# Kernel optimization log

Hardware: AMD Instinct MI355X
Metric: run time of the kernel (lower is better)

The kernel has to match this reference:

```python
import jax, jax.numpy as jnp
import numpy as np

D_MODEL = 512
HEADS = 8
FF_HIDDEN = 1024
EPS = 1e-6


def setup_inputs() -> dict:
    key = jax.random.key(0)
    ks = jax.random.split(key, 12)
    s = 1.0 / np.sqrt(D_MODEL)
    inp = {
        'x': jax.random.normal(ks[0], (2, 4096, D_MODEL), dtype=jnp.float32),
        'Wq': jax.random.normal(ks[1], (D_MODEL, D_MODEL), dtype=jnp.float32) * s,
        'bq': jnp.zeros((D_MODEL,), jnp.float32),
        'Wk': jax.random.normal(ks[2], (D_MODEL, D_MODEL), dtype=jnp.float32) * s,
        'bk': jnp.zeros((D_MODEL,), jnp.float32),
        'Wv': jax.random.normal(ks[3], (D_MODEL, D_MODEL), dtype=jnp.float32) * s,
        'bv': jnp.zeros((D_MODEL,), jnp.float32),
        'Wo': jax.random.normal(ks[4], (D_MODEL, D_MODEL), dtype=jnp.float32) * s,
        'bo': jnp.zeros((D_MODEL,), jnp.float32),
        'a1': jnp.ones((D_MODEL,), jnp.float32),
        'b1': jnp.zeros((D_MODEL,), jnp.float32),
        'a2': jnp.ones((D_MODEL,), jnp.float32),
        'b2': jnp.zeros((D_MODEL,), jnp.float32),
        'W1': jax.random.normal(ks[5], (D_MODEL, FF_HIDDEN), dtype=jnp.float32) * s,
        'c1': jnp.zeros((FF_HIDDEN,), jnp.float32),
        'W2': jax.random.normal(ks[6], (FF_HIDDEN, D_MODEL), dtype=jnp.float32) * (1.0 / np.sqrt(FF_HIDDEN)),
        'c2': jnp.zeros((D_MODEL,), jnp.float32),
    }
    return inp


def _layer_norm(x, a, b):
    # Faithful to source: uses unbiased std (torch default) and divides by (std + eps)
    mean = jnp.mean(x, axis=-1, keepdims=True)
    std = jnp.std(x, axis=-1, keepdims=True, ddof=1)
    return a * ((x - mean) / (std + EPS)) + b


def _encoder_block(x, Wq, bq, Wk, bk, Wv, bv, Wo, bo, a1, b1, a2, b2, W1, c1, W2, c2):
    B, S, D = x.shape
    H, dk = HEADS, D // HEADS
    q = (x @ Wq + bq).reshape(B, S, H, dk).transpose(0, 2, 1, 3)  # [B,H,S,dk]
    k = (x @ Wk + bk).reshape(B, S, H, dk).transpose(0, 2, 1, 3)
    v = (x @ Wv + bv).reshape(B, S, H, dk).transpose(0, 2, 1, 3)
    scores = jnp.einsum('bhqd,bhkd->bhqk', q, k) / np.sqrt(dk)
    probs = jax.nn.softmax(scores, axis=-1)
    attn = jnp.einsum('bhqk,bhkd->bhqd', probs, v)
    concat = attn.transpose(0, 2, 1, 3).reshape(B, S, D)
    attn_out = concat @ Wo + bo
    x = _layer_norm(x + attn_out, a1, b1)  # dropout = identity (eval mode)
    ffn = jax.nn.relu(x @ W1 + c1) @ W2 + c2
    return _layer_norm(x + ffn, a2, b2)


def reference(x, Wq, bq, Wk, bk, Wv, bv, Wo, bo, a1, b1, a2, b2, W1, c1, W2, c2):
    return _encoder_block(x, Wq, bq, Wk, bk, Wv, bv, Wo, bo, a1, b1, a2, b2, W1, c1, W2, c2)
```

## Files before the change

### kernel.cpp

```cpp
#include <hip/hip_runtime.h>
#include <stdint.h>

typedef short short8 __attribute__((ext_vector_type(8)));
typedef short short4v __attribute__((ext_vector_type(4)));
typedef float f32x4 __attribute__((ext_vector_type(4)));
typedef float f32x16 __attribute__((ext_vector_type(16)));
typedef unsigned int u32x4 __attribute__((ext_vector_type(4)));

#define LOG2E 1.44269504088896f
#define QSCALE (0.125f * LOG2E)

__device__ __forceinline__ unsigned short f2b(float f) {
  union { float f; unsigned int u; } x; x.f = f;
  unsigned int u = x.u;
  unsigned int r = (u + 0x7fffu + ((u >> 16) & 1u)) >> 16;
  return (unsigned short)r;
}
__device__ __forceinline__ float b2f(unsigned short s) {
  union { unsigned int u; float f; } x; x.u = ((unsigned int)s) << 16;
  return x.f;
}
__device__ __forceinline__ void gl16(const void* g, void* l) {
  __builtin_amdgcn_global_load_lds((const __attribute__((address_space(1))) void*)g,
                                   (__attribute__((address_space(3))) void*)l, 16, 0, 0);
}
__device__ __forceinline__ unsigned int cvtpk(float lo, float hi) {
  unsigned int r;
  asm("v_cvt_pk_bf16_f32 %0, %1, %2" : "=v"(r) : "v"(lo), "v"(hi));
  return r;
}
__device__ __forceinline__ void plswap(unsigned int& a, unsigned int& b) {
  asm volatile("v_permlane32_swap_b32 %0, %1" : "+v"(a), "+v"(b));
}

__global__ __launch_bounds__(256) void prep_k(
    const float* __restrict__ X, unsigned short* __restrict__ Xb,
    const float* __restrict__ Wq, const float* __restrict__ Wk,
    const float* __restrict__ Wv, const float* __restrict__ Wo,
    const float* __restrict__ W1, const float* __restrict__ W2,
    unsigned short* __restrict__ WqkvT, unsigned short* __restrict__ WoT,
    unsigned short* __restrict__ W1T, unsigned short* __restrict__ W2T,
    const float* __restrict__ bq, const float* __restrict__ bk,
    const float* __restrict__ bv, float* __restrict__ Bqkv) {
  __shared__ float t[64][65];
  int bid = blockIdx.x, tid = threadIdx.x;
  if (bid < 2048) {
    int i = bid * 256 + tid;
    const float* p = X + (size_t)i * 8;
    float4 a = *(const float4*)(p);
    float4 b = *(const float4*)(p + 4);
    short8 o;
    o[0] = (short)f2b(a.x); o[1] = (short)f2b(a.y);
    o[2] = (short)f2b(a.z); o[3] = (short)f2b(a.w);
    o[4] = (short)f2b(b.x); o[5] = (short)f2b(b.y);
    o[6] = (short)f2b(b.z); o[7] = (short)f2b(b.w);
    *(short8*)(Xb + (size_t)i * 8) = o;
    return;
  }
  if (bid == 2560) {
    for (int i = tid; i < 1536; i += 256) {
      float v = (i < 512) ? bq[i] * QSCALE : (i < 1024 ? bk[i - 512] : bv[i - 1024]);
      Bqkv[i] = v;
    }
    return;
  }
  int idx = bid - 2048;
  const float* W; unsigned short* WT; int K, N, kb, nb; float scale = 1.0f;
  if (idx < 256) {
    int sec = idx >> 6, local = idx & 63;
    K = 512; N = 512; kb = local >> 3; nb = local & 7;
    if (sec == 0) { W = Wq; WT = WqkvT; scale = QSCALE; }
    else if (sec == 1) { W = Wk; WT = WqkvT + 512 * 512; }
    else if (sec == 2) { W = Wv; WT = WqkvT + 2 * 512 * 512; }
    else { W = Wo; WT = WoT; }
  } else if (idx < 384) {
    int local = idx - 256; K = 512; N = 1024; kb = local >> 4; nb = local & 15;
    W = W1; WT = W1T;
  } else {
    int local = idx - 384; K = 1024; N = 512; kb = local >> 3; nb = local & 7;
    W = W2; WT = W2T;
  }
  int k0 = kb * 64, n0 = nb * 64;
  for (int i = tid; i < 4096; i += 256) {
    int r = i >> 6, c = i & 63;
    t[r][c] = W[(size_t)(k0 + r) * N + n0 + c];
  }
  __syncthreads();
  for (int i = tid; i < 4096; i += 256) {
    int r = i >> 6, c = i & 63;
    WT[(size_t)(n0 + r) * K + k0 + c] = f2b(t[c][r] * scale);
  }
}

template <int EPI>
__global__ __launch_bounds__(256) void gemm_bt(
    const unsigned short* __restrict__ A, const unsigned short* __restrict__ BT,
    const float* __restrict__ bias, float* __restrict__ Cf,
    unsigned short* __restrict__ Cb, int M, int N, int K) {
  __shared__ unsigned short As[2][128 * 32];
  __shared__ unsigned short Bs[2][128 * 32];
  int t = threadIdx.x, w = t >> 6, l = t & 63;
  int linb = blockIdx.x + gridDim.x * blockIdx.y;
  int q8 = (gridDim.x * gridDim.y) >> 3;
  int wk = (linb & 7) * q8 + (linb >> 3);
  int bm = wk / gridDim.y, bn = wk % gridDim.y;
  int wm = w >> 1, wn = w & 1;
  int g = l >> 4, ln = l & 15;
  f32x4 acc[4][4] = {};
  const unsigned short* Arow = A + (size_t)bm * 128 * K;
  const unsigned short* Brow = BT + (size_t)bn * 128 * K;
  int nk = K >> 5;

  auto stageg = [&](int buf, int kt) {
    int k0 = kt * 32;
#pragma unroll
    for (int i = 0; i < 2; ++i) {
      int cl = i * 256 + t;
      int r = cl >> 2, c = cl & 3;
      char* ldsA = (char*)&As[buf][0] + (size_t)(i * 256 + w * 64) * 16;
      char* ldsB = (char*)&Bs[buf][0] + (size_t)(i * 256 + w * 64) * 16;
      gl16(Arow + (size_t)r * K + k0 + c * 8, ldsA);
      gl16(Brow + (size_t)r * K + k0 + c * 8, ldsB);
    }
  };

  stageg(0, 0);
  for (int kt = 0; kt < nk; ++kt) {
    int cur = kt & 1;
    if (kt + 1 < nk) {
      stageg(cur ^ 1, kt + 1);
      asm volatile("s_waitcnt vmcnt(4)" ::: "memory");
    } else {
      asm volatile("s_waitcnt vmcnt(0)" ::: "memory");
    }
    __builtin_amdgcn_s_barrier();
    __builtin_amdgcn_sched_barrier(0);
    short8 af[4], bf[4];
    int ko = g * 8;
#pragma unroll
    for (int i = 0; i < 4; ++i)
      af[i] = *(const short8*)&As[cur][(wm * 64 + i * 16 + ln) * 32 + ko];
#pragma unroll
    for (int j = 0; j < 4; ++j)
      bf[j] = *(const short8*)&Bs[cur][(wn * 64 + j * 16 + ln) * 32 + ko];
    __builtin_amdgcn_s_setprio(1);
#pragma unroll
    for (int i = 0; i < 4; ++i)
#pragma unroll
      for (int j = 0; j < 4; ++j)
        acc[i][j] = __builtin_amdgcn_mfma_f32_16x16x32_bf16(af[i], bf[j], acc[i][j], 0, 0, 0);
    __builtin_amdgcn_s_setprio(0);
    __builtin_amdgcn_s_barrier();
  }
#pragma unroll
  for (int i = 0; i < 4; ++i) {
    int row = bm * 128 + wm * 64 + i * 16 + g * 4;
#pragma unroll
    for (int j = 0; j < 4; ++j) {
      int col = bn * 128 + wn * 64 + j * 16 + ln;
      float bv = bias[col];
      float vv[4];
#pragma unroll
      for (int r = 0; r < 4; ++r) {
        float v = acc[i][j][r] + bv;
        if constexpr (EPI == 2) v = v > 0.f ? v : 0.f;
        vv[r] = v;
      }
      if constexpr (EPI == 3) {
        if (col < 1024) {
#pragma unroll
          for (int r = 0; r < 4; ++r)
            Cb[(size_t)(col >> 9) * 4194304 + (size_t)(row + r) * 512 + (col & 511)] = f2b(vv[r]);
        } else {
          short4v pk;
#pragma unroll
          for (int r = 0; r < 4; ++r) pk[r] = (short)f2b(vv[r]);
          *(short4v*)((unsigned short*)Cf +
                      (size_t)((row >> 12) * 512 + (col & 511)) * 4096 + (row & 4095)) = pk;
        }
      } else {
#pragma unroll
        for (int r = 0; r < 4; ++r)
          Cb[(size_t)(row + r) * N + col] = f2b(vv[r]);
      }
    }
  }
}

template <int AMODE, bool WB>
__global__ __launch_bounds__(512) void gemmln_k(
    const unsigned short* __restrict__ A, const unsigned short* __restrict__ BT,
    const float* __restrict__ bias, const float* __restrict__ X,
    const float* __restrict__ gamma, const float* __restrict__ beta,
    float* __restrict__ outf, unsigned short* __restrict__ outb,
    const unsigned short* __restrict__ Opart, const float* __restrict__ L,
    int K) {
  __shared__ unsigned short As[AMODE ? 32 * 520 : 2 * 32 * 32];
  __shared__ unsigned short Bs[2][512 * 32];
  __shared__ float stats[8][32][2];
  __shared__ float minv[32][2];
  __shared__ float sli[8][32];
  int tid = threadIdx.x, wv = tid >> 6, lane = tid & 63;
  int g = lane >> 4, ln = lane & 15;
  int bm = blockIdx.x;
  int row0 = bm * 32;
  f32x4 acc[2][4] = {};

  if constexpr (AMODE == 1) {
    int b = row0 >> 12;
    int q0 = row0 & 4095;
    if (tid < 256) {
      int h = tid >> 5, qq = tid & 31;
      int bh = b * 8 + h;
      float s = L[(size_t)bh * 4096 + q0 + qq] + L[(size_t)(16 + bh) * 4096 + q0 + qq];
      sli[h][qq] = 1.0f / s;
    }
    __syncthreads();
    int col = tid;
    int h = col >> 6, d = col & 63;
    int bh = b * 8 + h;
    const unsigned short* p0 = Opart + (size_t)bh * 262144 + (size_t)d * 4096 + q0;
    const unsigned short* p1 = Opart + (size_t)(16 + bh) * 262144 + (size_t)d * 4096 + q0;
#pragma unroll
    for (int i = 0; i < 4; ++i) {
      short8 a = *(const short8*)(p0 + i * 8);
      short8 c = *(const short8*)(p1 + i * 8);
#pragma unroll
      for (int j = 0; j < 8; ++j) {
        int qq = i * 8 + j;
        float s = (b2f((unsigned short)a[j]) + b2f((unsigned short)c[j])) * sli[h][qq];
        As[qq * 520 + col] = f2b(s);
      }
    }
    __syncthreads();
  }

  const unsigned short* Arow = (AMODE == 0) ? (A + (size_t)bm * 32 * K) : nullptr;
  int nk = K >> 5;

  auto stageg = [&](int buf, int kt) {
    int k0 = kt * 32;
    if constexpr (AMODE == 0) {
      if (tid < 128) {
        int r = tid >> 2, c = tid & 3;
        gl16(Arow + (size_t)r * K + k0 + c * 8, (char*)As + (size_t)buf * 2048 + tid * 16);
      }
    }
#pragma unroll
    for (int i = 0; i < 4; ++i) {
      int u = i * 512 + tid;
      int r = u >> 2, c = u & 3;
      gl16(BT + (size_t)r * K + k0 + c * 8, (char*)&Bs[buf][0] + (size_t)u * 16);
    }
  };

  stageg(0, 0);
  for (int kt = 0; kt < nk; ++kt) {
    int cur = kt & 1;
    if (kt + 1 < nk) {
      stageg(cur ^ 1, kt + 1);
      if constexpr (AMODE == 0) {
        if (wv < 2) asm volatile("s_waitcnt vmcnt(5)" ::: "memory");
        else        asm volatile("s_waitcnt vmcnt(4)" ::: "memory");
      } else {
        asm volatile("s_waitcnt vmcnt(4)" ::: "memory");
      }
    } else {
      asm volatile("s_waitcnt vmcnt(0)" ::: "memory");
    }
    __builtin_amdgcn_s_barrier();
    __builtin_amdgcn_sched_barrier(0);
    int k0 = kt * 32;
    short8 af[2], bf[4];
#pragma unroll
    for (int i = 0; i < 2; ++i) {
      if constexpr (AMODE == 1)
        af[i] = *(const short8*)&As[(i * 16 + ln) * 520 + k0 + g * 8];
      else
        af[i] = *(const short8*)&As[cur * 1024 + (i * 16 + ln) * 32 + g * 8];
    }
#pragma unroll
    for (int j = 0; j < 4; ++j)
      bf[j] = *(const short8*)&Bs[cur][(wv * 64 + j * 16 + ln) * 32 + g * 8];
    __builtin_amdgcn_s_setprio(1);
#pragma unroll
    for (int i = 0; i < 2; ++i)
#pragma unroll
      for (int j = 0; j < 4; ++j)
        acc[i][j] = __builtin_amdgcn_mfma_f32_16x16x32_bf16(af[i], bf[j], acc[i][j], 0, 0, 0);
    __builtin_amdgcn_s_setprio(0);
    __builtin_amdgcn_s_barrier();
  }
  float v[2][4][4];
  float ps[8], pss[8];
#pragma unroll
  for (int k = 0; k < 8; ++k) { ps[k] = 0.f; pss[k] = 0.f; }
#pragma unroll
  for (int i = 0; i < 2; ++i)
#pragma unroll
    for (int j = 0; j < 4; ++j) {
      int col = wv * 64 + j * 16 + ln;
      float bv = bias[col];
#pragma unroll
      for (int r = 0; r < 4; ++r) {
        int row = i * 16 + g * 4 + r;
        float t = acc[i][j][r] + bv + X[(size_t)(row0 + row) * 512 + col];
        v[i][j][r] = t;
        ps[i * 4 + r] += t; pss[i * 4 + r] += t * t;
      }
    }
#pragma unroll
  for (int off = 1; off < 16; off <<= 1) {
#pragma unroll
    for (int k = 0; k < 8; ++k) {
      ps[k] += __shfl_xor(ps[k], off);
      pss[k] += __shfl_xor(pss[k], off);
    }
  }
  if (ln == 0) {
#pragma unroll
    for (int i = 0; i < 2; ++i)
#pragma unroll
      for (int r = 0; r < 4; ++r) {
        stats[wv][i * 16 + g * 4 + r][0] = ps[i * 4 + r];
        stats[wv][i * 16 + g * 4 + r][1] = pss[i * 4 + r];
      }
  }
  __syncthreads();
  if (tid < 32) {
    float S = 0.f, SS = 0.f;
#pragma unroll
    for (int w2 = 0; w2 < 8; ++w2) { S += stats[w2][tid][0]; SS += stats[w2][tid][1]; }
    float mean = S * (1.f / 512.f);
    float var = fmaxf((SS - 512.f * mean * mean) * (1.f / 511.f), 0.f);
    minv[tid][0] = mean;
    minv[tid][1] = 1.f / (sqrtf(var) + 1e-6f);
  }
  __syncthreads();
#pragma unroll
  for (int i = 0; i < 2; ++i)
#pragma unroll
    for (int j = 0; j < 4; ++j) {
      int col = wv * 64 + j * 16 + ln;
      float gm = gamma[col], bt2 = beta[col];
#pragma unroll
      for (int r = 0; r < 4; ++r) {
        int row = i * 16 + g * 4 + r;
        float o = gm * ((v[i][j][r] - minv[row][0]) * minv[row][1]) + bt2;
        outf[(size_t)(row0 + row) * 512 + col] = o;
        if constexpr (WB) outb[(size_t)(row0 + row) * 512 + col] = f2b(o);
      }
    }
}

__global__ __launch_bounds__(256, 2) void attn_k(
    const unsigned short* __restrict__ Q, const unsigned short* __restrict__ Kb,
    const unsigned short* __restrict__ Vt, unsigned short* __restrict__ Opart,
    float* __restrict__ L) {
  __shared__ unsigned short Ks[2][4096];
  __shared__ unsigned short Vs[3][4096];
  int tid = threadIdx.x, wv = tid >> 6, lane = tid & 63;
  int l31 = lane & 31, hi = lane >> 5;
  int lin = blockIdx.x + 16 * blockIdx.y + 256 * blockIdx.z;
  int wk = (lin & 7) * 64 + (lin >> 3);
  int qb = wk & 15, bh = (wk >> 4) & 15, z = wk >> 8;
  int b = bh >> 3, h = bh & 7;
  int q0 = qb * 256 + wv * 64;
  int kvbase = z * 2048;

  short8 qfA[4], qfB[4];
  {
    const unsigned short* qpA = Q + (size_t)(b * 4096 + q0 + l31) * 512 + h * 64;
    const unsigned short* qpB = qpA + 32 * 512;
#pragma unroll
    for (int ks = 0; ks < 4; ++ks) {
      qfA[ks] = *(const short8*)(qpA + ks * 16 + hi * 8);
      qfB[ks] = *(const short8*)(qpB + ks * 16 + hi * 8);
    }
  }

  short8 ones;
#pragma unroll
  for (int j = 0; j < 8; ++j) ones[j] = (short)0x3F80;

  const f32x16 Z = {};
  f32x16 oA0 = {}, oA1 = {}, oB0 = {}, oB1 = {}, laccA = {}, laccB = {};

  int skk[2], sc[2];
#pragma unroll
  for (int i = 0; i < 2; ++i) {
    int u = i * 256 + tid;
    int r2 = u >> 4, s = u & 15;
    skk[i] = 2 * r2 + (s & 1);
    sc[i] = ((s >> 1) ^ (r2 & 7)) * 8;
  }

  auto stage = [&](char* kb_lds, char* vb_lds, int kv) {
    const unsigned short* ksrc = Kb + (size_t)(b * 4096 + kv) * 512 + h * 64;
    const unsigned short* vsrc = Vt + (size_t)(bh * 64) * 4096 + kv;
#pragma unroll
    for (int i = 0; i < 2; ++i) {
      gl16(ksrc + (size_t)skk[i] * 512 + sc[i], kb_lds + (size_t)(i * 256 + wv * 64) * 16);
      gl16(vsrc + (size_t)skk[i] * 4096 + sc[i], vb_lds + (size_t)(i * 256 + wv * 64) * 16);
    }
  };

  int r2a = l31 >> 1, par = l31 & 1, perm = r2a & 7;
  int rdb = r2a * 256 + (par << 4);

  auto qk = [&](const char* kbase, f32x16& sA0, f32x16& sA1, f32x16& sB0, f32x16& sB1) {
    __builtin_amdgcn_s_setprio(1);
#pragma unroll
    for (int ks = 0; ks < 4; ++ks) {
      int c16 = ks * 2 + hi;
      int byteA = rdb + (((c16 ^ perm) << 1) << 4);
      short8 k0 = *(const short8*)(kbase + byteA);
      short8 k1 = *(const short8*)(kbase + byteA + 4096);
      if (ks == 0) {
        sA0 = __builtin_amdgcn_mfma_f32_32x32x16_bf16(k0, qfA[0], Z, 0, 0, 0);
        sA1 = __builtin_amdgcn_mfma_f32_32x32x16_bf16(k1, qfA[0], Z, 0, 0, 0);
        sB0 = __builtin_amdgcn_mfma_f32_32x32x16_bf16(k0, qfB[0], Z, 0, 0, 0);
        sB1 = __builtin_amdgcn_mfma_f32_32x32x16_bf16(k1, qfB[0], Z, 0, 0, 0);
      } else {
        sA0 = __builtin_amdgcn_mfma_f32_32x32x16_bf16(k0, qfA[ks], sA0, 0, 0, 0);
        sA1 = __builtin_amdgcn_mfma_f32_32x32x16_bf16(k1, qfA[ks], sA1, 0, 0, 0);
        sB0 = __builtin_amdgcn_mfma_f32_32x32x16_bf16(k0, qfB[ks], sB0, 0, 0, 0);
        sB1 = __builtin_amdgcn_mfma_f32_32x32x16_bf16(k1, qfB[ks], sB1, 0, 0, 0);
      }
    }
    __builtin_amdgcn_s_setprio(0);
  };

  auto pv = [&](const char* vbase, const short8* pfA, const short8* pfB) {
    __builtin_amdgcn_s_setprio(1);
#pragma unroll
    for (int ks = 0; ks < 4; ++ks) {
      int c16 = ks * 2 + hi;
      int byteA = rdb + (((c16 ^ perm) << 1) << 4);
      short8 v0 = *(const short8*)(vbase + byteA);
      short8 v1 = *(const short8*)(vbase + byteA + 4096);
      oA0 = __builtin_amdgcn_mfma_f32_32x32x16_bf16(v0, pfA[ks], oA0, 0, 0, 0);
      oA1 = __builtin_amdgcn_mfma_f32_32x32x16_bf16(v1, pfA[ks], oA1, 0, 0, 0);
      oB0 = __builtin_amdgcn_mfma_f32_32x32x16_bf16(v0, pfB[ks], oB0, 0, 0, 0);
      oB1 = __builtin_amdgcn_mfma_f32_32x32x16_bf16(v1, pfB[ks], oB1, 0, 0, 0);
      laccA = __builtin_amdgcn_mfma_f32_32x32x16_bf16(ones, pfA[ks], laccA, 0, 0, 0);
      laccB = __builtin_amdgcn_mfma_f32_32x32x16_bf16(ones, pfB[ks], laccB, 0, 0, 0);
    }
    __builtin_amdgcn_s_setprio(0);
  };

  auto exppack = [&](f32x16& s0, f32x16& s1, short8* pf) {
#pragma unroll
    for (int r = 0; r < 16; ++r) s0[r] = __builtin_amdgcn_exp2f(s0[r]);
#pragma unroll
    for (int r = 0; r < 16; ++r) s1[r] = __builtin_amdgcn_exp2f(s1[r]);
    unsigned int u0 = cvtpk(s0[0], s0[1]), u1 = cvtpk(s0[4], s0[5]);
    plswap(u0, u1);
    unsigned int u2 = cvtpk(s0[2], s0[3]), u3 = cvtpk(s0[6], s0[7]);
    plswap(u2, u3);
    unsigned int u4 = cvtpk(s0[8], s0[9]), u5 = cvtpk(s0[12], s0[13]);
    plswap(u4, u5);
    unsigned int u6 = cvtpk(s0[10], s0[11]), u7 = cvtpk(s0[14], s0[15]);
    plswap(u6, u7);
    union { u32x4 u; short8 s; } cv;
    cv.u = (u32x4){u0, u2, u1, u3}; pf[0] = cv.s;
    cv.u = (u32x4){u4, u6, u5, u7}; pf[1] = cv.s;
    unsigned int w0 = cvtpk(s1[0], s1[1]), w1 = cvtpk(s1[4], s1[5]);
    plswap(w0, w1);
    unsigned int w2 = cvtpk(s1[2], s1[3]), w3 = cvtpk(s1[6], s1[7]);
    plswap(w2, w3);
    unsigned int w4 = cvtpk(s1[8], s1[9]), w5 = cvtpk(s1[12], s1[13]);
    plswap(w4, w5);
    unsigned int w6 = cvtpk(s1[10], s1[11]), w7 = cvtpk(s1[14], s1[15]);
    plswap(w6, w7);
    cv.u = (u32x4){w0, w2, w1, w3}; pf[2] = cv.s;
    cv.u = (u32x4){w4, w6, w5, w7}; pf[3] = cv.s;
  };

  char* k0b = (char*)&Ks[0][0];
  char* k1b = (char*)&Ks[1][0];
  char* vA = (char*)&Vs[0][0];
  char* vB = (char*)&Vs[1][0];
  char* vC = (char*)&Vs[2][0];
  stage(k0b, vA, kvbase);
  __syncthreads();
  stage(k1b, vB, kvbase + 64);

  f32x16 sA0, sA1, sB0, sB1;
  qk(k0b, sA0, sA1, sB0, sB1);
  short8 pfA[4], pfB[4];
  exppack(sA0, sA1, pfA);
  exppack(sB0, sB1, pfB);

#pragma unroll 1
  for (int t = 1; t < 32; ++t) {
    __syncthreads();
    char* kr = (t & 1) ? k1b : k0b;
    char* kw = (t & 1) ? k0b : k1b;
    if (t < 31) stage(kw, vC, kvbase + (t + 1) * 64);
    qk(kr, sA0, sA1, sB0, sB1);
    pv(vA, pfA, pfB);
    exppack(sA0, sA1, pfA);
    exppack(sB0, sB1, pfB);
    char* tmp = vA; vA = vB; vB = vC; vC = tmp;
  }
  pv(vA, pfA, pfB);

  int plane = z * 16 + bh;
  unsigned short* op = Opart + (size_t)plane * 262144;
  int qA = q0 + l31, qB = q0 + 32 + l31;
#pragma unroll
  for (int r = 0; r < 16; ++r) {
    int dr = (r & 3) + 8 * (r >> 2) + 4 * hi;
    op[(size_t)dr * 4096 + qA] = f2b(oA0[r]);
    op[(size_t)(dr + 32) * 4096 + qA] = f2b(oA1[r]);
    op[(size_t)dr * 4096 + qB] = f2b(oB0[r]);
    op[(size_t)(dr + 32) * 4096 + qB] = f2b(oB1[r]);
  }
  if (hi == 0) {
    L[(size_t)plane * 4096 + qA] = laccA[0];
    L[(size_t)plane * 4096 + qB] = laccB[0];
  }
}

extern "C" void kernel_launch(void* const* d_in, const int* in_sizes, int n_in,
                              void* d_out, int out_size, void* d_ws, size_t ws_size,
                              hipStream_t stream) {
  const float* x  = (const float*)d_in[0];
  const float* Wq = (const float*)d_in[1];
  const float* bq = (const float*)d_in[2];
  const float* Wk = (const float*)d_in[3];
  const float* bk = (const float*)d_in[4];
  const float* Wv = (const float*)d_in[5];
  const float* bv = (const float*)d_in[6];
  const float* Wo = (const float*)d_in[7];
  const float* bo = (const float*)d_in[8];
  const float* a1 = (const float*)d_in[9];
  const float* b1 = (const float*)d_in[10];
  const float* a2 = (const float*)d_in[11];
  const float* b2 = (const float*)d_in[12];
  const float* W1 = (const float*)d_in[13];
  const float* c1 = (const float*)d_in[14];
  const float* W2 = (const float*)d_in[15];
  const float* c2 = (const float*)d_in[16];

  char* ws = (char*)d_ws;
  const size_t MB = 1024 * 1024;
  unsigned short* Xb  = (unsigned short*)(ws + 0);
  unsigned short* Qb  = (unsigned short*)(ws + 8 * MB);
  unsigned short* Kbf = (unsigned short*)(ws + 16 * MB);
  float* L = (float*)(ws + 24 * MB);
  unsigned short* Vtb = (unsigned short*)(ws + 32 * MB);
  unsigned short* WqkvT = (unsigned short*)(ws + 40 * MB);
  unsigned short* WoT = (unsigned short*)(ws + 41 * MB + 512 * 1024);
  unsigned short* W1T = (unsigned short*)(ws + 42 * MB);
  unsigned short* W2T = (unsigned short*)(ws + 43 * MB);
  unsigned short* Opart = (unsigned short*)(ws + 44 * MB);
  float* Bqkv = (float*)(ws + 44 * MB);
  float* Y1 = (float*)(ws + 60 * MB);
  unsigned short* Y1b = Qb;
  unsigned short* Hb  = Kbf;

  prep_k<<<2561, 256, 0, stream>>>(x, Xb, Wq, Wk, Wv, Wo, W1, W2,
                                   WqkvT, WoT, W1T, W2T, bq, bk, bv, Bqkv);

  gemm_bt<3><<<dim3(64, 12), 256, 0, stream>>>(Xb, WqkvT, Bqkv, (float*)Vtb, Qb, 8192, 1536, 512);

  attn_k<<<dim3(16, 16, 2), 256, 0, stream>>>(Qb, Kbf, Vtb, Opart, L);

  gemmln_k<1, true><<<256, 512, 0, stream>>>(nullptr, WoT, bo, x, a1, b1, Y1, Y1b,
                                             Opart, L, 512);
  gemm_bt<2><<<dim3(64, 8), 256, 0, stream>>>(Y1b, W1T, c1, nullptr, Hb, 8192, 1024, 512);
  gemmln_k<0, false><<<256, 512, 0, stream>>>(Hb, W2T, c2, Y1, a2, b2, (float*)d_out, nullptr,
                                              nullptr, nullptr, 1024);
}
```

Measured before the change: 188.2 us.

## Triple-buffer gemm_bt and halve gemmln_k threads with wider per-wave tiles

gemm_bt now uses a three-stage LDS ring, prefetching two K-tiles ahead, to hide more global load latency. gemmln_k drops from 512 to 256 threads, with each wave covering 128 columns (8 MFMA tiles). The AMODE=1 path uses an XOR-swizzled A tile in LDS instead of padding, and single-buffers B with a full wait each iteration. That last choice gives up load/compute overlap in the output-projection GEMM in exchange for less LDS use, and the wider tiles raise register pressure.

```diff
diff --git a/kernel.cpp b/kernel.cpp
--- a/kernel.cpp
+++ b/kernel.cpp
@@ -97,8 +97,8 @@
     const unsigned short* __restrict__ A, const unsigned short* __restrict__ BT,
     const float* __restrict__ bias, float* __restrict__ Cf,
     unsigned short* __restrict__ Cb, int M, int N, int K) {
-  __shared__ unsigned short As[2][128 * 32];
-  __shared__ unsigned short Bs[2][128 * 32];
+  __shared__ unsigned short As[3][128 * 32];
+  __shared__ unsigned short Bs[3][128 * 32];
   int t = threadIdx.x, w = t >> 6, l = t & 63;
   int linb = blockIdx.x + gridDim.x * blockIdx.y;
   int q8 = (gridDim.x * gridDim.y) >> 3;
@@ -125,10 +125,13 @@
   };
 
   stageg(0, 0);
+  stageg(1, 1);
+  int cur = 0, sbuf = 2;
   for (int kt = 0; kt < nk; ++kt) {
-    int cur = kt & 1;
-    if (kt + 1 < nk) {
-      stageg(cur ^ 1, kt + 1);
+    if (kt + 2 < nk) {
+      stageg(sbuf, kt + 2);
+      asm volatile("s_waitcnt vmcnt(8)" ::: "memory");
+    } else if (kt + 1 < nk) {
       asm volatile("s_waitcnt vmcnt(4)" ::: "memory");
     } else {
       asm volatile("s_waitcnt vmcnt(0)" ::: "memory");
@@ -151,6 +154,9 @@
         acc[i][j] = __builtin_amdgcn_mfma_f32_16x16x32_bf16(af[i], bf[j], acc[i][j], 0, 0, 0);
     __builtin_amdgcn_s_setprio(0);
     __builtin_amdgcn_s_barrier();
+    int old = cur;
+    cur = (cur == 2) ? 0 : cur + 1;
+    sbuf = old;
   }
 #pragma unroll
   for (int i = 0; i < 4; ++i) {
@@ -188,48 +194,51 @@
 }
 
 template <int AMODE, bool WB>
-__global__ __launch_bounds__(512) void gemmln_k(
+__global__ __launch_bounds__(256) void gemmln_k(
     const unsigned short* __restrict__ A, const unsigned short* __restrict__ BT,
     const float* __restrict__ bias, const float* __restrict__ X,
     const float* __restrict__ gamma, const float* __restrict__ beta,
     float* __restrict__ outf, unsigned short* __restrict__ outb,
     const unsigned short* __restrict__ Opart, const float* __restrict__ L,
     int K) {
-  __shared__ unsigned short As[AMODE ? 32 * 520 : 2 * 32 * 32];
-  __shared__ unsigned short Bs[2][512 * 32];
-  __shared__ float stats[8][32][2];
+  __shared__ unsigned short As[AMODE ? 32 * 512 : 2 * 32 * 32];
+  __shared__ unsigned short Bs[AMODE ? 512 * 32 : 2 * 512 * 32];
+  __shared__ float stats[4][32][2];
   __shared__ float minv[32][2];
   __shared__ float sli[8][32];
   int tid = threadIdx.x, wv = tid >> 6, lane = tid & 63;
   int g = lane >> 4, ln = lane & 15;
   int bm = blockIdx.x;
   int row0 = bm * 32;
-  f32x4 acc[2][4] = {};
+  f32x4 acc[2][8] = {};
 
   if constexpr (AMODE == 1) {
     int b = row0 >> 12;
     int q0 = row0 & 4095;
-    if (tid < 256) {
+    {
       int h = tid >> 5, qq = tid & 31;
       int bh = b * 8 + h;
       float s = L[(size_t)bh * 4096 + q0 + qq] + L[(size_t)(16 + bh) * 4096 + q0 + qq];
       sli[h][qq] = 1.0f / s;
     }
     __syncthreads();
-    int col = tid;
-    int h = col >> 6, d = col & 63;
-    int bh = b * 8 + h;
-    const unsigned short* p0 = Opart + (size_t)bh * 262144 + (size_t)d * 4096 + q0;
-    const unsigned short* p1 = Opart + (size_t)(16 + bh) * 262144 + (size_t)d * 4096 + q0;
-#pragma unroll
-    for (int i = 0; i < 4; ++i) {
-      short8 a = *(const short8*)(p0 + i * 8);
-      short8 c = *(const short8*)(p1 + i * 8);
-#pragma unroll
-      for (int j = 0; j < 8; ++j) {
-        int qq = i * 8 + j;
-        float s = (b2f((unsigned short)a[j]) + b2f((unsigned short)c[j])) * sli[h][qq];
-        As[qq * 520 + col] = f2b(s);
+#pragma unroll
+    for (int cc = 0; cc < 2; ++cc) {
+      int col = cc * 256 + tid;
+      int h = col >> 6, d = col & 63;
+      int bh = b * 8 + h;
+      const unsigned short* p0 = Opart + (size_t)bh * 262144 + (size_t)d * 4096 + q0;
+      const unsigned short* p1 = Opart + (size_t)(16 + bh) * 262144 + (size_t)d * 4096 + q0;
+#pragma unroll
+      for (int i = 0; i < 4; ++i) {
+        short8 a = *(const short8*)(p0 + i * 8);
+        short8 c = *(const short8*)(p1 + i * 8);
+#pragma unroll
+        for (int j = 0; j < 8; ++j) {
+          int qq = i * 8 + j;
+          float s = (b2f((unsigned short)a[j]) + b2f((unsigned short)c[j])) * sli[h][qq];
+          As[qq * 512 + (col ^ ((qq & 7) << 3))] = f2b(s);
+        }
       }
     }
     __syncthreads();
@@ -247,59 +256,65 @@
       }
     }
 #pragma unroll
-    for (int i = 0; i < 4; ++i) {
-      int u = i * 512 + tid;
+    for (int i = 0; i < 8; ++i) {
+      int u = i * 256 + tid;
       int r = u >> 2, c = u & 3;
-      gl16(BT + (size_t)r * K + k0 + c * 8, (char*)&Bs[buf][0] + (size_t)u * 16);
+      gl16(BT + (size_t)r * K + k0 + c * 8,
+           (char*)Bs + (AMODE ? 0 : (size_t)buf * 32768) + (size_t)u * 16);
     }
   };
 
-  stageg(0, 0);
+  if constexpr (AMODE == 0) stageg(0, 0);
   for (int kt = 0; kt < nk; ++kt) {
     int cur = kt & 1;
-    if (kt + 1 < nk) {
-      stageg(cur ^ 1, kt + 1);
-      if constexpr (AMODE == 0) {
-        if (wv < 2) asm volatile("s_waitcnt vmcnt(5)" ::: "memory");
-        else        asm volatile("s_waitcnt vmcnt(4)" ::: "memory");
+    if constexpr (AMODE == 1) {
+      stageg(0, kt);
+      asm volatile("s_waitcnt vmcnt(0)" ::: "memory");
+    } else {
+      if (kt + 1 < nk) {
+        stageg(cur ^ 1, kt + 1);
+        if (wv < 2) asm volatile("s_waitcnt vmcnt(9)" ::: "memory");
+        else        asm volatile("s_waitcnt vmcnt(8)" ::: "memory");
       } else {
-        asm volatile("s_waitcnt vmcnt(4)" ::: "memory");
-      }
-    } else {
-      asm volatile("s_waitcnt vmcnt(0)" ::: "memory");
+        asm volatile("s_waitcnt vmcnt(0)" ::: "memory");
+      }
     }
     __builtin_amdgcn_s_barrier();
     __builtin_amdgcn_sched_barrier(0);
     int k0 = kt * 32;
-    short8 af[2], bf[4];
+    short8 af[2], bf[8];
 #pragma unroll
     for (int i = 0; i < 2; ++i) {
-      if constexpr (AMODE == 1)
-        af[i] = *(const short8*)&As[(i * 16 + ln) * 520 + k0 + g * 8];
-      else
-        af[i] = *(const short8*)&As[cur * 1024 + (i * 16 + ln) * 32 + g * 8];
-    }
-#pragma unroll
-    for (int j = 0; j < 4; ++j)
-      bf[j] = *(const short8*)&Bs[cur][(wv * 64 + j * 16 + ln) * 32 + g * 8];
+      int row = i * 16 + ln;
+      if constexpr (AMODE == 1) {
+        int c16 = (k0 >> 3) + g;
+        af[i] = *(const short8*)&As[row * 512 + ((c16 ^ (row & 7)) << 3)];
+      } else {
+        af[i] = *(const short8*)&As[cur * 1024 + row * 32 + g * 8];
+      }
+    }
+#pragma unroll
+    for (int j = 0; j < 8; ++j)
+      bf[j] = *(const short8*)&Bs[(AMODE ? 0 : cur * 16384) +
+                                  (wv * 128 + j * 16 + ln) * 32 + g * 8];
     __builtin_amdgcn_s_setprio(1);
 #pragma unroll
     for (int i = 0; i < 2; ++i)
 #pragma unroll
-      for (int j = 0; j < 4; ++j)
+      for (int j = 0; j < 8; ++j)
         acc[i][j] = __builtin_amdgcn_mfma_f32_16x16x32_bf16(af[i], bf[j], acc[i][j], 0, 0, 0);
     __builtin_amdgcn_s_setprio(0);
     __builtin_amdgcn_s_barrier();
   }
-  float v[2][4][4];
+  float v[2][8][4];
   float ps[8], pss[8];
 #pragma unroll
   for (int k = 0; k < 8; ++k) { ps[k] = 0.f; pss[k] = 0.f; }
 #pragma unroll
   for (int i = 0; i < 2; ++i)
 #pragma unroll
-    for (int j = 0; j < 4; ++j) {
-      int col = wv * 64 + j * 16 + ln;
+    for (int j = 0; j < 8; ++j) {
+      int col = wv * 128 + j * 16 + ln;
       float bv = bias[col];
 #pragma unroll
       for (int r = 0; r < 4; ++r) {
@@ -330,7 +345,7 @@
   if (tid < 32) {
     float S = 0.f, SS = 0.f;
 #pragma unroll
-    for (int w2 = 0; w2 < 8; ++w2) { S += stats[w2][tid][0]; SS += stats[w2][tid][1]; }
+    for (int w2 = 0; w2 < 4; ++w2) { S += stats[w2][tid][0]; SS += stats[w2][tid][1]; }
     float mean = S * (1.f / 512.f);
     float var = fmaxf((SS - 512.f * mean * mean) * (1.f / 511.f), 0.f);
     minv[tid][0] = mean;
@@ -340,8 +355,8 @@
 #pragma unroll
   for (int i = 0; i < 2; ++i)
 #pragma unroll
-    for (int j = 0; j < 4; ++j) {
-      int col = wv * 64 + j * 16 + ln;
+    for (int j = 0; j < 8; ++j) {
+      int col = wv * 128 + j * 16 + ln;
       float gm = gamma[col], bt2 = beta[col];
 #pragma unroll
       for (int r = 0; r < 4; ++r) {
@@ -568,9 +583,9 @@
 
   attn_k<<<dim3(16, 16, 2), 256, 0, stream>>>(Qb, Kbf, Vtb, Opart, L);
 
-  gemmln_k<1, true><<<256, 512, 0, stream>>>(nullptr, WoT, bo, x, a1, b1, Y1, Y1b,
+  gemmln_k<1, true><<<256, 256, 0, stream>>>(nullptr, WoT, bo, x, a1, b1, Y1, Y1b,
                                              Opart, L, 512);
   gemm_bt<2><<<dim3(64, 8), 256, 0, stream>>>(Y1b, W1T, c1, nullptr, Hb, 8192, 1024, 512);
-  gemmln_k<0, false><<<256, 512, 0, stream>>>(Hb, W2T, c2, Y1, a2, b2, (float*)d_out, nullptr,
+  gemmln_k<0, false><<<256, 256, 0, stream>>>(Hb, W2T, c2, Y1, a2, b2, (float*)d_out, nullptr,
                                               nullptr, nullptr, 1024);
 }
```

Measured after the change: 193.6 us. 2.9% more time.
